# Kernel optimization log

Hardware: AMD Instinct MI355X
Metric: run time of the kernel (lower is better)

The kernel has to match this reference:

```python
import jax, jax.numpy as jnp
import numpy as np

B, T, E, D = 8, 2048, 2048, 256  # batch, seq (== max_seq_len), embed_size, block_size

def setup_inputs() -> dict:
    key = jax.random.key(0)
    kx, kq, kk, kv = jax.random.split(key, 4)
    x = jax.random.normal(kx, (B, T, E), dtype=jnp.float32)
    s = 1.0 / np.sqrt(E)
    Wq = jax.random.normal(kq, (E, D), dtype=jnp.float32) * s
    Wk = jax.random.normal(kk, (E, D), dtype=jnp.float32) * s
    Wv = jax.random.normal(kv, (E, D), dtype=jnp.float32) * s
    return {"x": x, "Wq": Wq, "Wk": Wk, "Wv": Wv}

def reference(x, Wq, Wk, Wv):
    # q,k,v: [B, T, D]
    q = jnp.einsum('bte,ed->btd', x, Wq)
    k = jnp.einsum('bte,ed->btd', x, Wk)
    v = jnp.einsum('bte,ed->btd', x, Wv)
    scores = jnp.einsum('bqd,bkd->bqk', q, k)  # [B, T, T]
    causal = jnp.tril(jnp.ones((T, T), dtype=bool))
    scores = jnp.where(causal, scores, -jnp.inf)
    inv_sqrt_d = 1.0 / np.sqrt(D).astype(np.float32)
    # Original divides by sqrt(D) twice: once before softmax, once inside -> net 1/D scale
    scores = scores * inv_sqrt_d
    attn = jax.nn.softmax(scores * inv_sqrt_d, axis=-1)
    z = jnp.einsum('bqk,bkd->bqd', attn, v)
    return z
```

## Files before the change

### kernel.cpp

```cpp
#include <hip/hip_runtime.h>
#include <hip/hip_bf16.h>

typedef unsigned short u16;
typedef unsigned int u32;
typedef __attribute__((ext_vector_type(8))) __bf16 bf16x8;
typedef __attribute__((ext_vector_type(4))) float f32x4;
typedef __attribute__((ext_vector_type(16))) float f32x16;
typedef __attribute__((ext_vector_type(2))) unsigned u32x2;
typedef __attribute__((ext_vector_type(4))) unsigned short u16x4;

__device__ __forceinline__ u16 f2bf(float f) {
  u32 u = __builtin_bit_cast(u32, f);
  return (u16)((u + 0x7fffu + ((u >> 16) & 1u)) >> 16);
}
__device__ __forceinline__ float bf2f(u16 h) {
  u32 u = ((u32)h) << 16;
  return __builtin_bit_cast(float, u);
}
__device__ __forceinline__ u32 pk2(float lo, float hi) {
  union { __bf16 b[2]; u32 u; } r;
  r.b[0] = (__bf16)lo; r.b[1] = (__bf16)hi;
  return r.u;
}

__device__ __forceinline__ void pl32pair(u32& a, u32& b) {
#if __has_builtin(__builtin_amdgcn_permlane32_swap)
  u32x2 r = __builtin_amdgcn_permlane32_swap(a, b, 0, 0);
  a = r.x; b = r.y;
#else
  int hi = (int)((threadIdx.x & 63) >> 5);
  u32 as = __shfl_xor(a, 32), bs = __shfl_xor(b, 32);
  u32 na = hi ? bs : a;
  u32 nb = hi ? b : as;
  a = na; b = nb;
#endif
}
__device__ __forceinline__ float red_max32(float x) {
  u32 a = __builtin_bit_cast(u32, x), b = __builtin_bit_cast(u32, x);
  pl32pair(a, b);
  return fmaxf(__builtin_bit_cast(float, a), __builtin_bit_cast(float, b));
}
__device__ __forceinline__ float red_sum32(float x) {
  u32 a = __builtin_bit_cast(u32, x), b = __builtin_bit_cast(u32, x);
  pl32pair(a, b);
  return __builtin_bit_cast(float, a) + __builtin_bit_cast(float, b);
}

__global__ void cast_w_kernel(const float* __restrict__ Wq, const float* __restrict__ Wk,
                              const float* __restrict__ Wv, u16* __restrict__ wbt) {
  __shared__ float tile[32][33];
  int e0 = blockIdx.x * 32, d0 = blockIdx.y * 32, w = blockIdx.z;
  const float* W = (w == 0) ? Wq : ((w == 1) ? Wk : Wv);
  int x = threadIdx.x, y = threadIdx.y;
#pragma unroll
  for (int j = 0; j < 4; j++)
    tile[y + j * 8][x] = W[(size_t)(e0 + y + j * 8) * 256 + d0 + x];
  __syncthreads();
#pragma unroll
  for (int j = 0; j < 4; j++)
    wbt[(size_t)(w * 256 + d0 + y + j * 8) * 2048 + e0 + x] = f2bf(tile[x][y + j * 8]);
}

__global__ __launch_bounds__(256, 2) void gemm_kernel(const float* __restrict__ X,
                                                      const u16* __restrict__ Bt,
                                                      u16* __restrict__ qbuf,
                                                      u16* __restrict__ kfrag,
                                                      u16* __restrict__ vfrag) {
  __shared__ __align__(16) u16 As[3][4096];
  __shared__ __align__(16) u16 Bs[3][6144];

  int tid = threadIdx.x;
  int w = tid >> 6, l = tid & 63;
  int lr = l & 15, lg = l >> 4;
  int wm = w >> 1, wn = w & 1;

  int bid = blockIdx.x;
  int xcd = bid & 7;
  int idx = bid >> 3;
  int rowb = xcd * 16 + (idx >> 2);
  int colb = idx & 3;
  int row0 = rowb * 128, col0 = colb * 192;

  int arow = w * 16 + (l >> 2);
  int achunk = l & 3;
  int aswz = achunk ^ ((l >> 3) & 3);
  const float* gax = X + (size_t)(row0 + arow) * 2048 + achunk * 8;
  float4 areg[2][2];

  int garow = w * 16 + (l >> 2);
  int scol = ((l & 3) * 8) ^ (((l >> 3) & 3) * 8);
  const u16* gb = Bt + (size_t)(col0 + garow) * 2048 + scol;

  f32x4 acc[4][6];
#pragma unroll
  for (int m = 0; m < 4; m++)
#pragma unroll
    for (int n = 0; n < 6; n++) acc[m][n] = (f32x4){0.f, 0.f, 0.f, 0.f};

  int rcol = (lg * 8) ^ (((lr >> 1) & 3) * 8);

#define LOAD_A(ts)                                                        \
  {                                                                       \
    _Pragma("unroll") for (int c = 0; c < 2; c++) {                       \
      const float* p = gax + (size_t)c * 64 * 2048 + (ts) * 32;           \
      areg[c][0] = *(const float4*)p;                                     \
      areg[c][1] = *(const float4*)(p + 4);                               \
    }                                                                     \
  }
#define WRITE_A(bi_)                                                      \
  {                                                                       \
    _Pragma("unroll") for (int c = 0; c < 2; c++) {                       \
      union { u16 h[8]; uint4 v; } oa;                                    \
      oa.h[0] = f2bf(areg[c][0].x); oa.h[1] = f2bf(areg[c][0].y);         \
      oa.h[2] = f2bf(areg[c][0].z); oa.h[3] = f2bf(areg[c][0].w);         \
      oa.h[4] = f2bf(areg[c][1].x); oa.h[5] = f2bf(areg[c][1].y);         \
      oa.h[6] = f2bf(areg[c][1].z); oa.h[7] = f2bf(areg[c][1].w);         \
      *(uint4*)&As[bi_][(c * 64 + arow) * 32 + aswz * 8] = oa.v;          \
    }                                                                     \
  }
#define STAGE_B3(ts, bi_)                                                 \
  {                                                                       \
    _Pragma("unroll") for (int c = 0; c < 3; c++)                         \
        __builtin_amdgcn_global_load_lds(                                 \
            (const __attribute__((address_space(1))) void*)(gb + (size_t)c * 64 * 2048 + (ts) * 32), \
            (__attribute__((address_space(3))) void*)&Bs[bi_][(c * 64 + w * 16) * 32], 16, 0, 0); \
  }

  LOAD_A(0);
  WRITE_A(0);
  LOAD_A(1);
  STAGE_B3(0, 0);
  STAGE_B3(1, 1);
  asm volatile("s_waitcnt vmcnt(3)" ::: "memory");
  asm volatile("s_waitcnt lgkmcnt(0)" ::: "memory");
  __builtin_amdgcn_s_barrier();

  int bi = 0, bn = 1, bp = 2;
  for (int t = 0; t < 64; t++) {
    int ts = (t + 2 <= 63) ? (t + 2) : 63;
    const u16* asb = As[bi];
    const u16* bsb = Bs[bi];

    bf16x8 bfr[6], af0, af1;
#pragma unroll
    for (int n = 0; n < 6; n++)
      bfr[n] = *(const bf16x8*)&bsb[(wn * 96 + n * 16 + lr) * 32 + rcol];
    af0 = *(const bf16x8*)&asb[(wm * 64 + 0 * 16 + lr) * 32 + rcol];
    af1 = *(const bf16x8*)&asb[(wm * 64 + 1 * 16 + lr) * 32 + rcol];
    WRITE_A(bn);
    LOAD_A(ts);
    __builtin_amdgcn_s_barrier();
    asm volatile("s_waitcnt lgkmcnt(0)" ::: "memory");
    __builtin_amdgcn_sched_barrier(0);
    __builtin_amdgcn_s_setprio(1);
#pragma unroll
    for (int n = 0; n < 6; n++) {
      acc[0][n] = __builtin_amdgcn_mfma_f32_16x16x32_bf16(af0, bfr[n], acc[0][n], 0, 0, 0);
      acc[1][n] = __builtin_amdgcn_mfma_f32_16x16x32_bf16(af1, bfr[n], acc[1][n], 0, 0, 0);
    }
    __builtin_amdgcn_s_setprio(0);
    __builtin_amdgcn_s_barrier();

    bf16x8 af2, af3;
    af2 = *(const bf16x8*)&asb[(wm * 64 + 2 * 16 + lr) * 32 + rcol];
    af3 = *(const bf16x8*)&asb[(wm * 64 + 3 * 16 + lr) * 32 + rcol];
    STAGE_B3(ts, bp);
    __builtin_amdgcn_s_barrier();
    asm volatile("s_waitcnt lgkmcnt(0)" ::: "memory");
    __builtin_amdgcn_sched_barrier(0);
    __builtin_amdgcn_s_setprio(1);
#pragma unroll
    for (int n = 0; n < 6; n++) {
      acc[2][n] = __builtin_amdgcn_mfma_f32_16x16x32_bf16(af2, bfr[n], acc[2][n], 0, 0, 0);
      acc[3][n] = __builtin_amdgcn_mfma_f32_16x16x32_bf16(af3, bfr[n], acc[3][n], 0, 0, 0);
    }
    __builtin_amdgcn_s_setprio(0);
    asm volatile("s_waitcnt vmcnt(7)" ::: "memory");
    __builtin_amdgcn_s_barrier();

    bi = (bi == 2) ? 0 : bi + 1;
    bn = (bn == 2) ? 0 : bn + 1;
    bp = (bp == 2) ? 0 : bp + 1;
  }
#undef LOAD_A
#undef WRITE_A
#undef STAGE_B3

  int crow = row0 + wm * 64;
#pragma unroll
  for (int m = 0; m < 4; m++) {
    int t0 = crow + m * 16 + lg * 4;
    int bb = t0 >> 11, tm0 = t0 & 2047;
#pragma unroll
    for (int n = 0; n < 6; n++) {
      int cb = col0 + wn * 96 + n * 16;
      int c = cb + lr;
      if (cb < 256) {
#pragma unroll
        for (int i = 0; i < 4; i++)
          qbuf[(size_t)(t0 + i) * 256 + c] = f2bf(acc[m][n][i]);
      } else if (cb < 512) {
        int kc = c - 256;
        int kvb = tm0 >> 5;
        int t16 = kc >> 4;
        int lhalf = (kc >> 3) & 1;
        int jj = kc & 7;
        size_t base = ((size_t)((bb * 64 + kvb) * 16 + t16) * 64 + lhalf * 32) * 8 + jj;
#pragma unroll
        for (int i = 0; i < 4; i++)
          kfrag[base + (size_t)((tm0 + i) & 31) * 8] = f2bf(acc[m][n][i]);
      } else {
        int vc = c - 512;
        int kvb = tm0 >> 5;
        int ch = (tm0 >> 4) & 1;
        int lhalf = (tm0 >> 3) & 1;
        int jj = tm0 & 7;
        int dblk = vc >> 5;
        int lane = (vc & 31) + lhalf * 32;
        size_t base = ((size_t)(((bb * 64 + kvb) * 2 + ch) * 8 + dblk) * 64 + lane) * 8 + jj;
        u16x4 pk = {f2bf(acc[m][n][0]), f2bf(acc[m][n][1]),
                    f2bf(acc[m][n][2]), f2bf(acc[m][n][3])};
        *(u16x4*)(vfrag + base) = pk;
      }
    }
  }
}

__global__ __launch_bounds__(512, 2) void attn_kernel(const u16* __restrict__ qbuf,
                                                      const u16* __restrict__ kfrag,
                                                      const u16* __restrict__ vfrag,
                                                      float* __restrict__ out) {
  __shared__ __align__(16) u16 qlds[16 * 512];
  __shared__ __align__(16) u16 klds[4 * 16 * 512];
  __shared__ float facc[32][264];
  __shared__ float sm[4][32];
  __shared__ float sl[4][32];

  int tid = threadIdx.x;
  int w = tid >> 6, l = tid & 63;
  int ql = l & 31, hi = l >> 5;
  int stream = w & 3, dhalf = w >> 2;
  int bid = blockIdx.x;
  int b = bid & 7;
  int p = bid >> 3;

  for (int tile = 0; tile < 2; tile++) {
    int jt = tile ? p : (63 - p);
    int q0 = jt * 32;

    if (tile) __syncthreads();
#pragma unroll
    for (int c = 0; c < 2; c++) {
      int m = c * 512 + tid;
      int t16 = m >> 6, ll = m & 63;
      const u16* src = qbuf + (size_t)(b * 2048 + q0 + (ll & 31)) * 256 + t16 * 16 + (ll >> 5) * 8;
      union { u16 h[8]; bf16x8 v; } in, ov;
      in.v = *(const bf16x8*)src;
#pragma unroll
      for (int j = 0; j < 8; j++) ov.h[j] = f2bf(bf2f(in.h[j]) * (1.0f / 256.0f));
      *(bf16x8*)&qlds[(t16 * 64 + ll) * 8] = ov.v;
    }
    __syncthreads();

    f32x16 o[4];
#pragma unroll
    for (int d = 0; d < 4; d++)
#pragma unroll
      for (int r = 0; r < 16; r++) o[d][r] = 0.f;
    float mreg = -__builtin_inff(), ell = 0.f;

    int nround = (jt >> 2) + 1;
    for (int rr = 0; rr < nround; rr++) {
      int jb = rr * 4 + stream;
      bool act = (jb <= jt);

      if (w < 4 && act) {
#pragma unroll
        for (int t = 0; t < 16; t++)
          __builtin_amdgcn_global_load_lds(
              (const __attribute__((address_space(1))) void*)(
                  kfrag + ((size_t)((b * 64 + jb) * 16 + t) * 64 + l) * 8),
              (__attribute__((address_space(3))) void*)&klds[(stream * 16 + t) * 512],
              16, 0, 0);
      }
      if (w < 4) asm volatile("s_waitcnt vmcnt(0)" ::: "memory");
      __syncthreads();

      if (act) {
        const u16* vb = vfrag + ((size_t)(b * 64 + jb) * 16 * 64 + l) * 8;
        bf16x8 ve0[4], ve1[4];
#pragma unroll
        for (int dd = 0; dd < 4; dd++) {
          ve0[dd] = *(const bf16x8*)(vb + (dhalf * 4 + dd) * 512);
          ve1[dd] = *(const bf16x8*)(vb + (8 + dhalf * 4 + dd) * 512);
        }

        const u16* kl = &klds[(stream * 16 * 64 + l) * 8];
        f32x16 sA, sB;
#pragma unroll
        for (int r = 0; r < 16; r++) { sA[r] = 0.f; sB[r] = 0.f; }
#pragma unroll
        for (int g = 0; g < 4; g++) {
          bf16x8 k0 = *(const bf16x8*)(kl + (g * 4 + 0) * 512);
          bf16x8 k1 = *(const bf16x8*)(kl + (g * 4 + 1) * 512);
          bf16x8 k2 = *(const bf16x8*)(kl + (g * 4 + 2) * 512);
          bf16x8 k3 = *(const bf16x8*)(kl + (g * 4 + 3) * 512);
          bf16x8 q0f = *(const bf16x8*)&qlds[((g * 4 + 0) * 64 + l) * 8];
          bf16x8 q1f = *(const bf16x8*)&qlds[((g * 4 + 1) * 64 + l) * 8];
          bf16x8 q2f = *(const bf16x8*)&qlds[((g * 4 + 2) * 64 + l) * 8];
          bf16x8 q3f = *(const bf16x8*)&qlds[((g * 4 + 3) * 64 + l) * 8];
          sA = __builtin_amdgcn_mfma_f32_32x32x16_bf16(k0, q0f, sA, 0, 0, 0);
          sB = __builtin_amdgcn_mfma_f32_32x32x16_bf16(k1, q1f, sB, 0, 0, 0);
          sA = __builtin_amdgcn_mfma_f32_32x32x16_bf16(k2, q2f, sA, 0, 0, 0);
          sB = __builtin_amdgcn_mfma_f32_32x32x16_bf16(k3, q3f, sB, 0, 0, 0);
        }

        float s[16];
#pragma unroll
        for (int r = 0; r < 16; r++) s[r] = sA[r] + sB[r];

        if (jb == jt) {
#pragma unroll
          for (int r = 0; r < 16; r++) {
            int kv = (r & 3) + 8 * (r >> 2) + 4 * hi;
            if (kv > ql) s[r] = -__builtin_inff();
          }
        }

        float mx = s[0];
#pragma unroll
        for (int r = 1; r < 16; r++) mx = fmaxf(mx, s[r]);
        mx = red_max32(mx);
        if (__any(mx > mreg + 8.f)) {
          float mnew = fmaxf(mreg, mx);
          float sf = __expf(mreg - mnew);
          mreg = mnew;
          ell *= sf;
#pragma unroll
          for (int d = 0; d < 4; d++)
#pragma unroll
            for (int r = 0; r < 16; r++) o[d][r] *= sf;
        }
        float pr[16], ps = 0.f;
#pragma unroll
        for (int r = 0; r < 16; r++) { pr[r] = __expf(s[r] - mreg); ps += pr[r]; }
        ell += red_sum32(ps);

        u32 wv[8];
#pragma unroll
        for (int i = 0; i < 8; i++) wv[i] = pk2(pr[2 * i], pr[2 * i + 1]);
        pl32pair(wv[0], wv[2]); pl32pair(wv[1], wv[3]);
        pl32pair(wv[4], wv[6]); pl32pair(wv[5], wv[7]);
        union { u32 u[4]; bf16x8 v; } B0, B1;
        B0.u[0] = wv[0]; B0.u[1] = wv[1]; B0.u[2] = wv[2]; B0.u[3] = wv[3];
        B1.u[0] = wv[4]; B1.u[1] = wv[5]; B1.u[2] = wv[6]; B1.u[3] = wv[7];

#pragma unroll
        for (int dd = 0; dd < 4; dd++) {
          o[dd] = __builtin_amdgcn_mfma_f32_32x32x16_bf16(ve0[dd], B0.v, o[dd], 0, 0, 0);
          o[dd] = __builtin_amdgcn_mfma_f32_32x32x16_bf16(ve1[dd], B1.v, o[dd], 0, 0, 0);
        }
      }
      __syncthreads();
    }

    if (w < 4 && l < 32) { sm[w][l] = mreg; sl[w][l] = ell; }
    __syncthreads();

    float M = fmaxf(fmaxf(sm[0][ql], sm[1][ql]), fmaxf(sm[2][ql], sm[3][ql]));
    float alpha = __expf(mreg - M);

#pragma unroll
    for (int ph = 0; ph < 4; ph++) {
      if (stream == ph) {
#pragma unroll
        for (int dd = 0; dd < 4; dd++)
#pragma unroll
          for (int rq = 0; rq < 4; rq++) {
            int base = (dhalf * 4 + dd) * 32 + 8 * rq + 4 * hi;
            f32x4 v;
#pragma unroll
            for (int i = 0; i < 4; i++) v[i] = alpha * o[dd][rq * 4 + i];
            float* fp = &facc[ql][base];
            if (ph == 0) *(f32x4*)fp = v;
            else {
              f32x4 old = *(const f32x4*)fp;
              *(f32x4*)fp = old + v;
            }
          }
      }
      __syncthreads();
    }

    int r = tid >> 4, lt = tid & 15;
    float Mr = fmaxf(fmaxf(sm[0][r], sm[1][r]), fmaxf(sm[2][r], sm[3][r]));
    float denom = 0.f;
#pragma unroll
    for (int ww = 0; ww < 4; ww++) denom += __expf(sm[ww][r] - Mr) * sl[ww][r];
    float inv = 1.0f / denom;
    float* orow = out + (size_t)(b * 2048 + q0 + r) * 256;
#pragma unroll
    for (int j = 0; j < 4; j++) {
      int c = (lt + j * 16) * 4;
      f32x4 v = *(const f32x4*)&facc[r][c];
      v[0] *= inv; v[1] *= inv; v[2] *= inv; v[3] *= inv;
      *(f32x4*)&orow[c] = v;
    }
  }
}

extern "C" void kernel_launch(void* const* d_in, const int* in_sizes, int n_in,
                              void* d_out, int out_size, void* d_ws, size_t ws_size,
                              hipStream_t stream) {
  (void)in_sizes; (void)n_in; (void)out_size; (void)ws_size;
  const float* x = (const float*)d_in[0];
  const float* Wq = (const float*)d_in[1];
  const float* Wk = (const float*)d_in[2];
  const float* Wv = (const float*)d_in[3];
  float* out = (float*)d_out;

  char* ws = (char*)d_ws;
  u16* wbt   = (u16*)(ws + 67108864);
  u16* qbuf  = (u16*)(ws + 70254592);
  u16* kfrag = (u16*)(ws + 78643200);
  u16* vfrag = (u16*)(ws + 87031808);

  cast_w_kernel<<<dim3(64, 8, 3), dim3(32, 8), 0, stream>>>(Wq, Wk, Wv, wbt);
  gemm_kernel<<<512, 256, 0, stream>>>(x, wbt, qbuf, kfrag, vfrag);
  attn_kernel<<<256, 512, 0, stream>>>(qbuf, kfrag, vfrag, out);
}
```

Measured before the change: 123.0 us.

## Double-buffer K tiles in LDS to prefetch the next round during compute

Allocates two LDS buffers for K fragments and issues the global-to-LDS load for the next round's K block right after the barrier, so it overlaps the current round's QK and PV MFMA work. The trailing per-round barrier is removed, because the leading barrier now guards buffer reuse. To fit the larger LDS footprint, the output accumulation scratch (facc) is aliased onto the first K buffer. The risks are higher LDS usage, which may limit occupancy, and the vmcnt(0) wait, which also waits on the V register loads.

```diff
diff --git a/kernel.cpp b/kernel.cpp
--- a/kernel.cpp
+++ b/kernel.cpp
@@ -231,10 +231,10 @@
                                                       const u16* __restrict__ vfrag,
                                                       float* __restrict__ out) {
   __shared__ __align__(16) u16 qlds[16 * 512];
-  __shared__ __align__(16) u16 klds[4 * 16 * 512];
-  __shared__ float facc[32][264];
+  __shared__ __align__(16) u16 klds2[2][4 * 16 * 512];
   __shared__ float sm[4][32];
   __shared__ float sl[4][32];
+  float (*facc)[264] = (float (*)[264]) & klds2[0][0];
 
   int tid = threadIdx.x;
   int w = tid >> 6, l = tid & 63;
@@ -244,6 +244,16 @@
   int b = bid & 7;
   int p = bid >> 3;
 
+#define STAGE_K(jb_, buf_)                                                           \
+  {                                                                                  \
+    _Pragma("unroll") for (int t = 0; t < 16; t++)                                   \
+        __builtin_amdgcn_global_load_lds(                                            \
+            (const __attribute__((address_space(1))) void*)(                         \
+                kfrag + ((size_t)((b * 64 + (jb_)) * 16 + t) * 64 + l) * 8),         \
+            (__attribute__((address_space(3))) void*)&klds2[buf_][(stream * 16 + t) * 512], \
+            16, 0, 0);                                                               \
+  }
+
   for (int tile = 0; tile < 2; tile++) {
     int jt = tile ? p : (63 - p);
     int q0 = jt * 32;
@@ -270,23 +280,20 @@
     float mreg = -__builtin_inff(), ell = 0.f;
 
     int nround = (jt >> 2) + 1;
+
+    if (w < 4 && stream <= jt) STAGE_K(stream, 0);
+
     for (int rr = 0; rr < nround; rr++) {
+      int cur = rr & 1;
       int jb = rr * 4 + stream;
-      bool act = (jb <= jt);
-
-      if (w < 4 && act) {
-#pragma unroll
-        for (int t = 0; t < 16; t++)
-          __builtin_amdgcn_global_load_lds(
-              (const __attribute__((address_space(1))) void*)(
-                  kfrag + ((size_t)((b * 64 + jb) * 16 + t) * 64 + l) * 8),
-              (__attribute__((address_space(3))) void*)&klds[(stream * 16 + t) * 512],
-              16, 0, 0);
-      }
+
       if (w < 4) asm volatile("s_waitcnt vmcnt(0)" ::: "memory");
       __syncthreads();
 
-      if (act) {
+      int jbn = jb + 4;
+      if (w < 4 && rr + 1 < nround && jbn <= jt) STAGE_K(jbn, cur ^ 1);
+
+      if (jb <= jt) {
         const u16* vb = vfrag + ((size_t)(b * 64 + jb) * 16 * 64 + l) * 8;
         bf16x8 ve0[4], ve1[4];
 #pragma unroll
@@ -295,7 +302,7 @@
           ve1[dd] = *(const bf16x8*)(vb + (8 + dhalf * 4 + dd) * 512);
         }
 
-        const u16* kl = &klds[(stream * 16 * 64 + l) * 8];
+        const u16* kl = &klds2[cur][(stream * 16 * 64 + l) * 8];
         f32x16 sA, sB;
 #pragma unroll
         for (int r = 0; r < 16; r++) { sA[r] = 0.f; sB[r] = 0.f; }
@@ -361,7 +368,6 @@
           o[dd] = __builtin_amdgcn_mfma_f32_32x32x16_bf16(ve1[dd], B1.v, o[dd], 0, 0, 0);
         }
       }
-      __syncthreads();
     }
 
     if (w < 4 && l < 32) { sm[w][l] = mreg; sl[w][l] = ell; }
@@ -407,6 +413,7 @@
       *(f32x4*)&orow[c] = v;
     }
   }
+#undef STAGE_K
 }
 
 extern "C" void kernel_launch(void* const* d_in, const int* in_sizes, int n_in,
```

Result: faster. 120.6 us, median of 6 (-2.0%).
